# Optimization experiments

Hardware: AMD Instinct MI355X
Metric: run time of the kernel (lower is better)

The kernel has to match this reference:

```python
import jax, jax.numpy as jnp
import numpy as np

B, N, FIN, FOUT = 8, 2048, 128, 128


def setup_inputs() -> dict:
    key = jax.random.key(0)
    k1, k2, k3, k4, k5 = jax.random.split(key, 5)
    x = jax.random.normal(k1, (B, N, FIN), dtype=jnp.float32)
    adj = jax.random.randint(k2, (N, N), 0, 2, dtype=jnp.int32)
    # W stored [in, out] (transpose of torch Linear weight; same math via x @ W)
    W = jax.random.normal(k3, (FIN, FOUT), dtype=jnp.float32) * (1.0 / np.sqrt(FIN))
    # a: Linear(2*out, 1) split into src/dst halves: a([h_i,h_j]) = h_i@a_src + h_j@a_dst
    a_src = jax.random.normal(k4, (FOUT,), dtype=jnp.float32) * 0.1
    a_dst = jax.random.normal(k5, (FOUT,), dtype=jnp.float32) * 0.1
    return {"x": x, "adj": adj, "W": W, "a_src": a_src, "a_dst": a_dst}


def reference(x, adj, W, a_src, a_dst):
    # h: [B, N, FOUT]
    h = jnp.einsum('bnf,fo->bno', x, W)
    # attention logits e_ij = LeakyReLU(a_src.h_i + a_dst.h_j), built by broadcast
    s_i = jnp.einsum('bno,o->bn', h, a_src)  # [B, N]
    s_j = jnp.einsum('bno,o->bn', h, a_dst)  # [B, N]
    e = jax.nn.leaky_relu(s_i[:, :, None] + s_j[:, None, :], negative_slope=0.2)  # [B,N,N]
    scores = jnp.where(adj[None, :, :] == 0, -jnp.inf, e)
    attn = jax.nn.softmax(scores, axis=-1)
    attn = jnp.nan_to_num(attn, nan=0.0)  # rows with no neighbors -> all zeros
    # dropout is identity in eval mode
    out = jnp.einsum('bij,bjo->bio', attn, h)  # [B, N, FOUT]
    return out
```

## Files before the change

### kernel.cpp

```cpp
#include <hip/hip_runtime.h>
#include <math.h>

#define BATCH 8
#define NN 2048
#define FF 128

typedef __attribute__((ext_vector_type(4))) float f32x4;
typedef _Float16 half8 __attribute__((ext_vector_type(8)));

__device__ __forceinline__ unsigned short h2u(_Float16 h) {
    return __builtin_bit_cast(unsigned short, h);
}

__global__ __launch_bounds__(256) void k_h(const float* __restrict__ x,
                                           const int* __restrict__ adj,
                                           const float* __restrict__ W,
                                           const float* __restrict__ a_src,
                                           const float* __restrict__ a_dst,
                                           unsigned short* __restrict__ hF,
                                           float* __restrict__ Eg,  float* __restrict__ E2g,
                                           float* __restrict__ Sg,  float* __restrict__ S2g,
                                           unsigned* __restrict__ amT) {
    __shared__ float sred[4 * 16];
    __shared__ float dred[4 * 16];

    const int t = threadIdx.x;
    const int w = t >> 6, lane = t & 63;
    const int nl = lane & 15, quad = lane >> 4;
    const int row0 = blockIdx.x * 16;
    const int b = row0 >> 11, jloc0 = row0 & 2047;
    const int gr = row0 + nl;
    const int nt0 = w * 2;

    {
        const int prow = blockIdx.x * 2 + (w >> 1);
        const int* __restrict__ ar = adj + (size_t)prow * NN;
        const int s0 = (w & 1) * 16;
        #pragma unroll
        for (int s = 0; s < 16; ++s) {
            const int seg = s0 + s;
            const unsigned long long m = __ballot(ar[seg * 64 + lane] != 0);
            if (lane == 0)  amT[(size_t)(seg * 2) * NN + prow] = (unsigned)m;
            if (lane == 32) amT[(size_t)(seg * 2 + 1) * NN + prow] = (unsigned)(m >> 32);
        }
    }

    f32x4 acc[2] = {{0.f,0.f,0.f,0.f},{0.f,0.f,0.f,0.f}};

    #pragma unroll
    for (int ks = 0; ks < 4; ++ks) {
        const float4 xa = *reinterpret_cast<const float4*>(&x[(size_t)gr * FF + ks * 32 + quad * 8]);
        const float4 xb = *reinterpret_cast<const float4*>(&x[(size_t)gr * FF + ks * 32 + quad * 8 + 4]);
        const float xv[8] = {xa.x, xa.y, xa.z, xa.w, xb.x, xb.y, xb.z, xb.w};
        half8 ah, al;
        #pragma unroll
        for (int i = 0; i < 8; ++i) {
            const _Float16 hh = (_Float16)xv[i];
            ah[i] = hh;
            al[i] = (_Float16)(xv[i] - (float)hh);
        }
        #pragma unroll
        for (int nn = 0; nn < 2; ++nn) {
            const float* __restrict__ wp = W + (size_t)(ks * 32 + quad * 8) * FF + (nt0 + nn) * 16 + nl;
            half8 bh, bl;
            #pragma unroll
            for (int j = 0; j < 8; ++j) {
                const float wv = wp[j * FF];
                const _Float16 hh = (_Float16)wv;
                bh[j] = hh;
                bl[j] = (_Float16)(wv - (float)hh);
            }
            acc[nn] = __builtin_amdgcn_mfma_f32_16x16x32_f16(ah, bh, acc[nn], 0, 0, 0);
            acc[nn] = __builtin_amdgcn_mfma_f32_16x16x32_f16(al, bh, acc[nn], 0, 0, 0);
            acc[nn] = __builtin_amdgcn_mfma_f32_16x16x32_f16(ah, bl, acc[nn], 0, 0, 0);
        }
    }

    const int jloc = jloc0 + quad * 4;
    const int jg = jloc >> 3, u0 = jloc & 7;
    #pragma unroll
    for (int nn = 0; nn < 2; ++nn) {
        ushort4 hv;
        hv.x = h2u((_Float16)acc[nn][0]);
        hv.y = h2u((_Float16)acc[nn][1]);
        hv.z = h2u((_Float16)acc[nn][2]);
        hv.w = h2u((_Float16)acc[nn][3]);
        *reinterpret_cast<ushort4*>(&hF[(size_t)b * 262144 + (nt0 + nn) * 32768 + jg * 128 + nl * 8 + u0]) = hv;
    }

    float as[2], ad[2];
    #pragma unroll
    for (int nn = 0; nn < 2; ++nn) {
        const int col = (nt0 + nn) * 16 + nl;
        as[nn] = a_src[col];
        ad[nn] = a_dst[col];
    }
    #pragma unroll
    for (int r = 0; r < 4; ++r) {
        float sp = acc[0][r] * as[0] + acc[1][r] * as[1];
        float dp = acc[0][r] * ad[0] + acc[1][r] * ad[1];
        #pragma unroll
        for (int off = 8; off >= 1; off >>= 1) {
            sp += __shfl_xor(sp, off, 16);
            dp += __shfl_xor(dp, off, 16);
        }
        if (nl == 0) {
            sred[w * 16 + quad * 4 + r] = sp;
            dred[w * 16 + quad * 4 + r] = dp;
        }
    }
    __syncthreads();
    if (t < 16) {
        const float sp = sred[t] + sred[16 + t] + sred[32 + t] + sred[48 + t];
        const float dp = dred[t] + dred[16 + t] + dred[32 + t] + dred[48 + t];
        const int row = row0 + t;
        Sg[row]  = __expf(sp - 2.f);
        S2g[row] = __expf(0.2f * sp - 2.f);
        Eg[row]  = __expf(dp - 2.f);
        E2g[row] = __expf(0.2f * dp - 2.f);
    }
}

__global__ __launch_bounds__(512, 4) void k_attn(const unsigned short* __restrict__ hF,
                                                 const unsigned* __restrict__ amT,
                                                 const float* __restrict__ Eg,
                                                 const float* __restrict__ E2g,
                                                 const float* __restrict__ Sg,
                                                 const float* __restrict__ S2g,
                                                 float* __restrict__ P,
                                                 float* __restrict__ L) {
    __shared__ unsigned short pA[2 * 64 * 72];

    const int t = threadIdx.x;
    const int b = blockIdx.y;
    const int i0 = blockIdx.x * 64;
    const int jh = blockIdx.z;
    const int jbase = jh * 1024;

    const int rp = t >> 4, jw4 = t & 15;
    const int ra = rp * 2, rb = ra + 1;
    const float Sa  = Sg[(size_t)b * NN + i0 + ra];
    const float S2a = S2g[(size_t)b * NN + i0 + ra];
    const float Sb  = Sg[(size_t)b * NN + i0 + rb];
    const float S2b = S2g[(size_t)b * NN + i0 + rb];
    const int bitb = (jw4 & 7) * 4;
    const int pwo = ra * 72 + jw4 * 4;
    const float* __restrict__ Egb  = Eg  + (size_t)b * NN + jbase;
    const float* __restrict__ E2gb = E2g + (size_t)b * NN + jbase;
    const unsigned* __restrict__ amb = amT + (size_t)(jh * 32) * NN + i0;

    const int w = t >> 6, lane = t & 63;
    const int nl = lane & 15, quad = lane >> 4;
    const int mtp = w & 1, ntp = w >> 1;
    const unsigned short* __restrict__ hFb = hF + (size_t)b * 262144;
    int bofs[2], aofs[2];
    #pragma unroll
    for (int nn = 0; nn < 2; ++nn) bofs[nn] = (ntp + nn * 4) * 32768 + (jbase + quad * 8) * 16 + nl * 8;
    #pragma unroll
    for (int mm = 0; mm < 2; ++mm) aofs[mm] = ((mtp + mm * 2) * 16 + nl) * 72 + quad * 8;

    f32x4 acc[2][2] = {{{0.f,0.f,0.f,0.f},{0.f,0.f,0.f,0.f}},{{0.f,0.f,0.f,0.f},{0.f,0.f,0.f,0.f}}};
    float la = 0.f, lb = 0.f;

    for (int tt = 0; tt < 16; ++tt) {
        const int buf = tt & 1;
        const int jofs = tt * 1024;

        half8 bfr[2][2];
        #pragma unroll
        for (int nn = 0; nn < 2; ++nn) {
            bfr[nn][0] = *reinterpret_cast<const half8*>(hFb + bofs[nn] + jofs);
            bfr[nn][1] = *reinterpret_cast<const half8*>(hFb + bofs[nn] + jofs + 512);
        }

        {
            const int jb = tt * 64 + jw4 * 4;
            const float4 ej4  = *reinterpret_cast<const float4*>(&Egb[jb]);
            const float4 e2j4 = *reinterpret_cast<const float4*>(&E2gb[jb]);
            const uint2 mw = *reinterpret_cast<const uint2*>(&amb[(size_t)(tt * 2 + (jw4 >> 3)) * NN + ra]);
            const float ejA[4]  = {ej4.x, ej4.y, ej4.z, ej4.w};
            const float e2jA[4] = {e2j4.x, e2j4.y, e2j4.z, e2j4.w};
            ushort4 ha, hb;
            #pragma unroll
            for (int jj = 0; jj < 4; ++jj) {
                const float ua = fmaxf(Sa * ejA[jj], S2a * e2jA[jj]);
                const float ub = fmaxf(Sb * ejA[jj], S2b * e2jA[jj]);
                const float pa = ((mw.x >> (bitb + jj)) & 1u) ? ua : 0.f;
                const float pb = ((mw.y >> (bitb + jj)) & 1u) ? ub : 0.f;
                la += pa;
                lb += pb;
                ((unsigned short*)&ha)[jj] = h2u((_Float16)pa);
                ((unsigned short*)&hb)[jj] = h2u((_Float16)pb);
            }
            *reinterpret_cast<ushort4*>(&pA[buf * 4608 + pwo]) = ha;
            *reinterpret_cast<ushort4*>(&pA[buf * 4608 + pwo + 72]) = hb;
        }

        __syncthreads();

        half8 afr[2][2];
        #pragma unroll
        for (int mm = 0; mm < 2; ++mm) {
            afr[mm][0] = *reinterpret_cast<const half8*>(&pA[buf * 4608 + aofs[mm]]);
            afr[mm][1] = *reinterpret_cast<const half8*>(&pA[buf * 4608 + aofs[mm] + 32]);
        }
        #pragma unroll
        for (int mm = 0; mm < 2; ++mm) {
            #pragma unroll
            for (int kh = 0; kh < 2; ++kh) {
                acc[mm][0] = __builtin_amdgcn_mfma_f32_16x16x32_f16(afr[mm][kh], bfr[0][kh], acc[mm][0], 0, 0, 0);
                acc[mm][1] = __builtin_amdgcn_mfma_f32_16x16x32_f16(afr[mm][kh], bfr[1][kh], acc[mm][1], 0, 0, 0);
            }
        }
    }

    #pragma unroll
    for (int off = 8; off >= 1; off >>= 1) {
        la += __shfl_xor(la, off, 16);
        lb += __shfl_xor(lb, off, 16);
    }

    float* __restrict__ Pb = P + ((size_t)jh * BATCH + b) * 262144;
    float* __restrict__ Lb = L + ((size_t)jh * BATCH + b) * 2048;
    if (jw4 == 0) {
        Lb[i0 + ra] = la;
        Lb[i0 + rb] = lb;
    }
    #pragma unroll
    for (int mm = 0; mm < 2; ++mm) {
        const int lrow = (mtp + mm * 2) * 16 + quad * 4;
        #pragma unroll
        for (int r = 0; r < 4; ++r) {
            #pragma unroll
            for (int nn = 0; nn < 2; ++nn) {
                const int col = (ntp + nn * 4) * 16 + nl;
                Pb[(size_t)(i0 + lrow + r) * FF + col] = acc[mm][nn][r];
            }
        }
    }
}

__global__ __launch_bounds__(256) void k_comb(const float* __restrict__ P,
                                              const float* __restrict__ L,
                                              float* __restrict__ out) {
    const int g0 = blockIdx.x * 512 + threadIdx.x;
    #pragma unroll
    for (int it = 0; it < 2; ++it) {
        const int g = g0 + it * 256;
        const size_t flat = (size_t)g * 4;
        const int row = (int)(flat >> 7);
        const float l = L[row] + L[16384 + row];
        const float inv = (l > 0.f) ? 1.f / l : 0.f;
        const float4 p0 = *reinterpret_cast<const float4*>(&P[flat]);
        const float4 p1 = *reinterpret_cast<const float4*>(&P[2097152 + flat]);
        *reinterpret_cast<float4*>(&out[flat]) =
            make_float4((p0.x + p1.x) * inv, (p0.y + p1.y) * inv,
                        (p0.z + p1.z) * inv, (p0.w + p1.w) * inv);
    }
}

extern "C" void kernel_launch(void* const* d_in, const int* in_sizes, int n_in,
                              void* d_out, int out_size, void* d_ws, size_t ws_size,
                              hipStream_t stream) {
    const float* x     = (const float*)d_in[0];
    const int*   adj   = (const int*)d_in[1];
    const float* W     = (const float*)d_in[2];
    const float* a_src = (const float*)d_in[3];
    const float* a_dst = (const float*)d_in[4];
    float* out = (float*)d_out;

    unsigned short* hF = (unsigned short*)d_ws;
    float* Eg  = (float*)(hF + 2097152);
    float* E2g = Eg + 16384;
    float* Sg  = E2g + 16384;
    float* S2g = Sg + 16384;
    unsigned* amT = (unsigned*)(S2g + 16384);
    float* P = (float*)(amT + 131072);
    float* L = P + 4194304;

    k_h<<<1024, 256, 0, stream>>>(x, adj, W, a_src, a_dst, hF, Eg, E2g, Sg, S2g, amT);
    k_attn<<<dim3(32, BATCH, 2), 512, 0, stream>>>(hF, amT, Eg, E2g, Sg, S2g, P, L);
    k_comb<<<1024, 256, 0, stream>>>(P, L, out);
}
```

Before: 111.5 us.

## Drop split-K over neighbors and fuse normalization into attention kernel

The attention kernel no longer splits the neighbor dimension across two blocks. Each block now handles 32 rows over all 2048 neighbors and writes the normalized output directly, so the partial-sum buffers and the separate combine kernel go away. This removes one launch and the fp32 round trip of the partial P and L arrays through global memory. In exchange each block runs twice as many loop iterations and does half the MFMA work per iteration, and the grid keeps the same 512 blocks.

Measured after the change: 114.1 us. +2.3%, slower.

```diff
diff --git a/kernel.cpp b/kernel.cpp
--- a/kernel.cpp
+++ b/kernel.cpp
@@ -127,42 +127,36 @@
                                                  const float* __restrict__ E2g,
                                                  const float* __restrict__ Sg,
                                                  const float* __restrict__ S2g,
-                                                 float* __restrict__ P,
-                                                 float* __restrict__ L) {
-    __shared__ unsigned short pA[2 * 64 * 72];
+                                                 float* __restrict__ out) {
+    __shared__ unsigned short pA[2 * 32 * 72];
+    __shared__ float lred[32];
 
     const int t = threadIdx.x;
     const int b = blockIdx.y;
-    const int i0 = blockIdx.x * 64;
-    const int jh = blockIdx.z;
-    const int jbase = jh * 1024;
-
-    const int rp = t >> 4, jw4 = t & 15;
-    const int ra = rp * 2, rb = ra + 1;
-    const float Sa  = Sg[(size_t)b * NN + i0 + ra];
-    const float S2a = S2g[(size_t)b * NN + i0 + ra];
-    const float Sb  = Sg[(size_t)b * NN + i0 + rb];
-    const float S2b = S2g[(size_t)b * NN + i0 + rb];
-    const int bitb = (jw4 & 7) * 4;
-    const int pwo = ra * 72 + jw4 * 4;
-    const float* __restrict__ Egb  = Eg  + (size_t)b * NN + jbase;
-    const float* __restrict__ E2gb = E2g + (size_t)b * NN + jbase;
-    const unsigned* __restrict__ amb = amT + (size_t)(jh * 32) * NN + i0;
+    const int i0 = blockIdx.x * 32;
+
+    const int rp = t >> 4, j4 = t & 15;
+    const float Sa  = Sg[(size_t)b * NN + i0 + rp];
+    const float S2a = S2g[(size_t)b * NN + i0 + rp];
+    const int bitb = (j4 & 7) * 4;
+    const int pwo = rp * 72 + j4 * 4;
+    const float* __restrict__ Egb  = Eg  + (size_t)b * NN;
+    const float* __restrict__ E2gb = E2g + (size_t)b * NN;
+    const unsigned* __restrict__ amb = amT + i0 + rp;
 
     const int w = t >> 6, lane = t & 63;
     const int nl = lane & 15, quad = lane >> 4;
     const int mtp = w & 1, ntp = w >> 1;
     const unsigned short* __restrict__ hFb = hF + (size_t)b * 262144;
-    int bofs[2], aofs[2];
-    #pragma unroll
-    for (int nn = 0; nn < 2; ++nn) bofs[nn] = (ntp + nn * 4) * 32768 + (jbase + quad * 8) * 16 + nl * 8;
-    #pragma unroll
-    for (int mm = 0; mm < 2; ++mm) aofs[mm] = ((mtp + mm * 2) * 16 + nl) * 72 + quad * 8;
-
-    f32x4 acc[2][2] = {{{0.f,0.f,0.f,0.f},{0.f,0.f,0.f,0.f}},{{0.f,0.f,0.f,0.f},{0.f,0.f,0.f,0.f}}};
-    float la = 0.f, lb = 0.f;
-
-    for (int tt = 0; tt < 16; ++tt) {
+    int bofs[2];
+    #pragma unroll
+    for (int nn = 0; nn < 2; ++nn) bofs[nn] = (ntp + nn * 4) * 32768 + quad * 128 + nl * 8;
+    const int aofs = (mtp * 16 + nl) * 72 + quad * 8;
+
+    f32x4 acc[2] = {{0.f,0.f,0.f,0.f},{0.f,0.f,0.f,0.f}};
+    float la = 0.f;
+
+    for (int tt = 0; tt < 32; ++tt) {
         const int buf = tt & 1;
         const int jofs = tt * 1024;
 
@@ -174,88 +168,50 @@
         }
 
         {
-            const int jb = tt * 64 + jw4 * 4;
+            const int jb = tt * 64 + j4 * 4;
             const float4 ej4  = *reinterpret_cast<const float4*>(&Egb[jb]);
             const float4 e2j4 = *reinterpret_cast<const float4*>(&E2gb[jb]);
-            const uint2 mw = *reinterpret_cast<const uint2*>(&amb[(size_t)(tt * 2 + (jw4 >> 3)) * NN + ra]);
+            const unsigned mw = amb[(size_t)(tt * 2 + (j4 >> 3)) * NN];
             const float ejA[4]  = {ej4.x, ej4.y, ej4.z, ej4.w};
             const float e2jA[4] = {e2j4.x, e2j4.y, e2j4.z, e2j4.w};
-            ushort4 ha, hb;
+            ushort4 ha;
             #pragma unroll
             for (int jj = 0; jj < 4; ++jj) {
                 const float ua = fmaxf(Sa * ejA[jj], S2a * e2jA[jj]);
-                const float ub = fmaxf(Sb * ejA[jj], S2b * e2jA[jj]);
-                const float pa = ((mw.x >> (bitb + jj)) & 1u) ? ua : 0.f;
-                const float pb = ((mw.y >> (bitb + jj)) & 1u) ? ub : 0.f;
+                const float pa = ((mw >> (bitb + jj)) & 1u) ? ua : 0.f;
                 la += pa;
-                lb += pb;
                 ((unsigned short*)&ha)[jj] = h2u((_Float16)pa);
-                ((unsigned short*)&hb)[jj] = h2u((_Float16)pb);
             }
-            *reinterpret_cast<ushort4*>(&pA[buf * 4608 + pwo]) = ha;
-            *reinterpret_cast<ushort4*>(&pA[buf * 4608 + pwo + 72]) = hb;
+            *reinterpret_cast<ushort4*>(&pA[buf * 2304 + pwo]) = ha;
         }
 
         __syncthreads();
 
-        half8 afr[2][2];
-        #pragma unroll
-        for (int mm = 0; mm < 2; ++mm) {
-            afr[mm][0] = *reinterpret_cast<const half8*>(&pA[buf * 4608 + aofs[mm]]);
-            afr[mm][1] = *reinterpret_cast<const half8*>(&pA[buf * 4608 + aofs[mm] + 32]);
-        }
-        #pragma unroll
-        for (int mm = 0; mm < 2; ++mm) {
-            #pragma unroll
-            for (int kh = 0; kh < 2; ++kh) {
-                acc[mm][0] = __builtin_amdgcn_mfma_f32_16x16x32_f16(afr[mm][kh], bfr[0][kh], acc[mm][0], 0, 0, 0);
-                acc[mm][1] = __builtin_amdgcn_mfma_f32_16x16x32_f16(afr[mm][kh], bfr[1][kh], acc[mm][1], 0, 0, 0);
-            }
-        }
-    }
-
-    #pragma unroll
-    for (int off = 8; off >= 1; off >>= 1) {
-        la += __shfl_xor(la, off, 16);
-        lb += __shfl_xor(lb, off, 16);
-    }
-
-    float* __restrict__ Pb = P + ((size_t)jh * BATCH + b) * 262144;
-    float* __restrict__ Lb = L + ((size_t)jh * BATCH + b) * 2048;
-    if (jw4 == 0) {
-        Lb[i0 + ra] = la;
-        Lb[i0 + rb] = lb;
-    }
-    #pragma unroll
-    for (int mm = 0; mm < 2; ++mm) {
-        const int lrow = (mtp + mm * 2) * 16 + quad * 4;
-        #pragma unroll
-        for (int r = 0; r < 4; ++r) {
-            #pragma unroll
-            for (int nn = 0; nn < 2; ++nn) {
-                const int col = (ntp + nn * 4) * 16 + nl;
-                Pb[(size_t)(i0 + lrow + r) * FF + col] = acc[mm][nn][r];
-            }
-        }
-    }
-}
-
-__global__ __launch_bounds__(256) void k_comb(const float* __restrict__ P,
-                                              const float* __restrict__ L,
-                                              float* __restrict__ out) {
-    const int g0 = blockIdx.x * 512 + threadIdx.x;
-    #pragma unroll
-    for (int it = 0; it < 2; ++it) {
-        const int g = g0 + it * 256;
-        const size_t flat = (size_t)g * 4;
-        const int row = (int)(flat >> 7);
-        const float l = L[row] + L[16384 + row];
+        half8 afr[2];
+        afr[0] = *reinterpret_cast<const half8*>(&pA[buf * 2304 + aofs]);
+        afr[1] = *reinterpret_cast<const half8*>(&pA[buf * 2304 + aofs + 32]);
+        #pragma unroll
+        for (int kh = 0; kh < 2; ++kh) {
+            acc[0] = __builtin_amdgcn_mfma_f32_16x16x32_f16(afr[kh], bfr[0][kh], acc[0], 0, 0, 0);
+            acc[1] = __builtin_amdgcn_mfma_f32_16x16x32_f16(afr[kh], bfr[1][kh], acc[1], 0, 0, 0);
+        }
+    }
+
+    #pragma unroll
+    for (int off = 8; off >= 1; off >>= 1) la += __shfl_xor(la, off, 16);
+    if (j4 == 0) lred[rp] = la;
+    __syncthreads();
+
+    float* __restrict__ ob = out + ((size_t)b * NN + i0) * FF;
+    #pragma unroll
+    for (int r = 0; r < 4; ++r) {
+        const int lr = mtp * 16 + quad * 4 + r;
+        const float l = lred[lr];
         const float inv = (l > 0.f) ? 1.f / l : 0.f;
-        const float4 p0 = *reinterpret_cast<const float4*>(&P[flat]);
-        const float4 p1 = *reinterpret_cast<const float4*>(&P[2097152 + flat]);
-        *reinterpret_cast<float4*>(&out[flat]) =
-            make_float4((p0.x + p1.x) * inv, (p0.y + p1.y) * inv,
-                        (p0.z + p1.z) * inv, (p0.w + p1.w) * inv);
+        #pragma unroll
+        for (int nn = 0; nn < 2; ++nn) {
+            ob[(size_t)lr * FF + (ntp + nn * 4) * 16 + nl] = acc[nn][r] * inv;
+        }
     }
 }
 
@@ -275,10 +231,7 @@
     float* Sg  = E2g + 16384;
     float* S2g = Sg + 16384;
     unsigned* amT = (unsigned*)(S2g + 16384);
-    float* P = (float*)(amT + 131072);
-    float* L = P + 4194304;
 
     k_h<<<1024, 256, 0, stream>>>(x, adj, W, a_src, a_dst, hF, Eg, E2g, Sg, S2g, amT);
-    k_attn<<<dim3(32, BATCH, 2), 512, 0, stream>>>(hF, amT, Eg, E2g, Sg, S2g, P, L);
-    k_comb<<<1024, 256, 0, stream>>>(P, L, out);
-}
+    k_attn<<<dim3(64, BATCH), 512, 0, stream>>>(hF, amT, Eg, E2g, Sg, S2g, out);
+}
```
